# Kernel tuning notes

Hardware: AMD Instinct MI355X
Metric: run time of the kernel (lower is better)

Reference implementation:

```python
import jax, jax.numpy as jnp
import numpy as np

DIM = 128
NUM_HEADS = 4
SPLIT_SIZE = 8
HEAD_DIM = DIM // NUM_HEADS
SCALE = HEAD_DIM ** -0.5


def setup_inputs() -> dict:
    key = jax.random.key(0)
    qkv = jax.random.normal(key, (3, 8, 4096, DIM), dtype=jnp.float32)
    return {"qkv": qkv, "H": 64, "W": 64}


def _to_windows(x, H, W, H_sp, W_sp):
    # x: [B, L, C] -> [B*nW, num_heads, H_sp*W_sp, head_dim]
    B, L, C = x.shape
    x = x.reshape(B, H // H_sp, H_sp, W // W_sp, W_sp, C)
    x = x.transpose(0, 1, 3, 2, 4, 5).reshape(-1, H_sp * W_sp, NUM_HEADS, C // NUM_HEADS)
    return x.transpose(0, 2, 1, 3)


def reference(qkv, H, W):
    # idx=0 branch: vertical strips, H_sp = H (full height), W_sp = split_size
    H_sp, W_sp = H, SPLIT_SIZE
    B, L, C = qkv.shape[1], qkv.shape[2], qkv.shape[3]
    q = _to_windows(qkv[0], H, W, H_sp, W_sp) * SCALE
    k = _to_windows(qkv[1], H, W, H_sp, W_sp)
    v = _to_windows(qkv[2], H, W, H_sp, W_sp)
    # [nW, h, S, S] with S = H_sp*W_sp
    attn = jax.nn.softmax(jnp.einsum('whqd,whkd->whqk', q, k), axis=-1)
    x = jnp.einsum('whqk,whkd->whqd', attn, v)
    # merge heads: [nW, S, C]
    x = x.transpose(0, 2, 1, 3).reshape(-1, H_sp * W_sp, C)
    # windows2img: [B, H*W, C]
    x = x.reshape(B, H // H_sp, W // W_sp, H_sp, W_sp, C)
    x = x.transpose(0, 1, 3, 2, 4, 5).reshape(B, H * W, C)
    return x
```

## Files before the change

kernel.cpp:

```cpp
#include <hip/hip_runtime.h>


typedef __attribute__((ext_vector_type(8)))  short bf16x8;
typedef __attribute__((ext_vector_type(4)))  float f32x4;
typedef __attribute__((ext_vector_type(16))) float f32x16;
typedef __attribute__((ext_vector_type(4)))  int   i32x4;

#define MFMA32(a, b, c) __builtin_amdgcn_mfma_f32_32x32x16_bf16(a, b, c, 0, 0, 0)

__device__ __forceinline__ unsigned cvtpk(float lo, float hi) {
    unsigned r;
    asm("v_cvt_pk_bf16_f32 %0, %1, %2" : "=v"(r) : "v"(lo), "v"(hi));
    return r;
}
__device__ __forceinline__ void plswap(unsigned& a, unsigned& b) {
    asm("v_permlane32_swap_b32 %0, %1" : "+v"(a), "+v"(b));
}

__global__ __launch_bounds__(256, 4)
void lepe_attn_r8(const float* __restrict__ qkv, float* __restrict__ out)
{
    __shared__ __align__(16) short    Ks[256 * 32];
    __shared__ __align__(16) unsigned Vt32[32 * 132];

    const int tid  = threadIdx.x;
    const int wave = tid >> 6;
    const int lane = tid & 63;
    const int m31  = lane & 31;
    const int hi   = lane >> 5;

    const int blk  = blockIdx.x;
    const int pair = blk >> 2;
    const int qsp  = blk & 3;
    const int wi   = pair >> 2;
    const int hd   = pair & 3;
    const int b    = wi >> 3;
    const int wb   = wi & 7;
    const int chead = hd * 32;

    const size_t baseQ = (size_t)b * 524288;
    const size_t baseK = baseQ + 8u * 524288;
    const size_t baseV = baseQ + 16u * 524288;

    const int q0w = qsp * 128 + wave * 32;
    const float QS = 0.17677669529663687f * 1.4426950408889634f;
    bf16x8 qf0, qf1;
    {
        int qg = q0w + m31;
        int lq = (qg >> 3) * 64 + wb * 8 + (qg & 7);
        const float* qp = qkv + baseQ + (size_t)lq * 128 + chead + hi * 8;
        f32x4 qa = *(const f32x4*)qp;
        f32x4 qb = *(const f32x4*)(qp + 4);
        f32x4 qc = *(const f32x4*)(qp + 16);
        f32x4 qd = *(const f32x4*)(qp + 20);
        i32x4 w0, w1;
        w0[0] = cvtpk(qa[0] * QS, qa[1] * QS);
        w0[1] = cvtpk(qa[2] * QS, qa[3] * QS);
        w0[2] = cvtpk(qb[0] * QS, qb[1] * QS);
        w0[3] = cvtpk(qb[2] * QS, qb[3] * QS);
        w1[0] = cvtpk(qc[0] * QS, qc[1] * QS);
        w1[1] = cvtpk(qc[2] * QS, qc[3] * QS);
        w1[2] = cvtpk(qd[0] * QS, qd[1] * QS);
        w1[3] = cvtpk(qd[2] * QS, qd[3] * QS);
        qf0 = __builtin_bit_cast(bf16x8, w0);
        qf1 = __builtin_bit_cast(bf16x8, w1);
    }

    f32x16 o = (f32x16)0.0f;
    float lsum = 0.0f;

    const short* Vts = (const short*)Vt32;

    for (int stage = 0; stage < 2; ++stage) {
        if (stage) __syncthreads();
        const int keybase = stage * 256;

#pragma unroll
        for (int i = 0; i < 4; ++i) {
            int chunk = i * 256 + tid;
            int row   = chunk >> 2;
            int part  = chunk & 3;
            int gk    = keybase + row;
            int lk    = (gk >> 3) * 64 + wb * 8 + (gk & 7);
            const float* kp = qkv + baseK + (size_t)lk * 128 + chead + part * 8;
            f32x4 k0 = *(const f32x4*)kp;
            f32x4 k1 = *(const f32x4*)(kp + 4);
            i32x4 kd;
            kd[0] = cvtpk(k0[0], k0[1]);
            kd[1] = cvtpk(k0[2], k0[3]);
            kd[2] = cvtpk(k1[0], k1[1]);
            kd[3] = cvtpk(k1[2], k1[3]);
            *(i32x4*)&Ks[row * 32 + ((part ^ ((row >> 1) & 3)) << 3)] = kd;
        }
        {
            int p    = tid >> 1;
            int half = tid & 1;
            int k0g  = keybase + 2 * p;
            int l0   = (k0g >> 3) * 64 + wb * 8 + (k0g & 7);
            const float* va = qkv + baseV + (size_t)l0 * 128 + chead + half * 16;
            const float* vb = va + 128;
            f32x4 a[4], bb[4];
#pragma unroll
            for (int j = 0; j < 4; ++j) { a[j] = *(const f32x4*)(va + 4 * j); bb[j] = *(const f32x4*)(vb + 4 * j); }
#pragma unroll
            for (int j = 0; j < 4; ++j)
#pragma unroll
                for (int e = 0; e < 4; ++e) {
                    int dim = half * 16 + j * 4 + e;
                    Vt32[dim * 132 + p] = cvtpk(a[j][e], bb[j][e]);
                }
        }
        __syncthreads();

        for (int kb = 0; kb < 256; kb += 32) {
            int row0 = kb + m31;
            int swz  = (row0 >> 1) & 3;
            bf16x8 kfa = *(const bf16x8*)&Ks[row0 * 32 + (((0 + hi) ^ swz) << 3)];
            bf16x8 kfb = *(const bf16x8*)&Ks[row0 * 32 + (((2 + hi) ^ swz) << 3)];
            bf16x8 vf0 = *(const bf16x8*)&Vts[m31 * 264 + kb + hi * 8];
            bf16x8 vf1 = *(const bf16x8*)&Vts[m31 * 264 + kb + 16 + hi * 8];

            f32x16 s = MFMA32(kfa, qf0, (f32x16)0.0f);
            s = MFMA32(kfb, qf1, s);

            float p[16];
#pragma unroll
            for (int r = 0; r < 16; ++r) p[r] = __builtin_amdgcn_exp2f(s[r]);

            float t01 = p[0] + p[1],   t23 = p[2] + p[3];
            float t45 = p[4] + p[5],   t67 = p[6] + p[7];
            float t89 = p[8] + p[9],   tab = p[10] + p[11];
            float tcd = p[12] + p[13], tef = p[14] + p[15];
            lsum += ((t01 + t23) + (t45 + t67)) + ((t89 + tab) + (tcd + tef));

            unsigned c0 = cvtpk(p[0], p[1]);
            unsigned c1 = cvtpk(p[2], p[3]);
            unsigned c2 = cvtpk(p[4], p[5]);
            unsigned c3 = cvtpk(p[6], p[7]);
            plswap(c0, c2);
            plswap(c1, c3);
            i32x4 pw0; pw0[0] = c0; pw0[1] = c1; pw0[2] = c2; pw0[3] = c3;

            unsigned c4 = cvtpk(p[8], p[9]);
            unsigned c5 = cvtpk(p[10], p[11]);
            unsigned c6 = cvtpk(p[12], p[13]);
            unsigned c7 = cvtpk(p[14], p[15]);
            plswap(c4, c6);
            plswap(c5, c7);
            i32x4 pw1; pw1[0] = c4; pw1[1] = c5; pw1[2] = c6; pw1[3] = c7;

            o = MFMA32(__builtin_bit_cast(bf16x8, pw0), vf0, o);
            o = MFMA32(__builtin_bit_cast(bf16x8, pw1), vf1, o);
        }
    }

    float ls  = lsum + __shfl_xor(lsum, 32);
    float inv = 1.0f / ls;
    const size_t baseO = (size_t)b * 524288;
#pragma unroll
    for (int r = 0; r < 16; ++r) {
        int qw = (r & 3) + 8 * (r >> 2) + 4 * hi;
        float iv = __shfl(inv, qw);
        int q  = q0w + qw;
        int lq = (q >> 3) * 64 + wb * 8 + (q & 7);
        out[baseO + (size_t)lq * 128 + chead + m31] = o[r] * iv;
    }
}

extern "C" void kernel_launch(void* const* d_in, const int* in_sizes, int n_in,
                              void* d_out, int out_size, void* d_ws, size_t ws_size,
                              hipStream_t stream) {
    const float* qkv = (const float*)d_in[0];
    float* out = (float*)d_out;
    lepe_attn_r8<<<dim3(1024), dim3(256), 0, stream>>>(qkv, out);
}
```

Before: 104.2 us.

## Merge four query-split blocks into one 1024-thread block sharing K/V tiles

The four blocks that handled different query quarters of the same window and head become one 1024-thread block of 16 waves. K and V for that window-head are now loaded from global memory, converted to bf16 and staged in shared memory once instead of four times, with the staging loops reshaped so each thread does less copying. The cost is larger blocks: 256 blocks, about one per CU, with every wave waiting at one block-wide barrier. The launch bound of 1024 threads and 4 blocks may also force a tight register budget and cause spills.

```diff
diff --git a/kernel.cpp b/kernel.cpp
--- a/kernel.cpp
+++ b/kernel.cpp
@@ -17,8 +17,8 @@
     asm("v_permlane32_swap_b32 %0, %1" : "+v"(a), "+v"(b));
 }
 
-__global__ __launch_bounds__(256, 4)
-void lepe_attn_r8(const float* __restrict__ qkv, float* __restrict__ out)
+__global__ __launch_bounds__(1024, 4)
+void lepe_attn_r9(const float* __restrict__ qkv, float* __restrict__ out)
 {
     __shared__ __align__(16) short    Ks[256 * 32];
     __shared__ __align__(16) unsigned Vt32[32 * 132];
@@ -29,9 +29,7 @@
     const int m31  = lane & 31;
     const int hi   = lane >> 5;
 
-    const int blk  = blockIdx.x;
-    const int pair = blk >> 2;
-    const int qsp  = blk & 3;
+    const int pair = blockIdx.x;
     const int wi   = pair >> 2;
     const int hd   = pair & 3;
     const int b    = wi >> 3;
@@ -42,7 +40,9 @@
     const size_t baseK = baseQ + 8u * 524288;
     const size_t baseV = baseQ + 16u * 524288;
 
-    const int q0w = qsp * 128 + wave * 32;
+    const int qsp = wave >> 2;
+    const int wv  = wave & 3;
+    const int q0w = qsp * 128 + wv * 32;
     const float QS = 0.17677669529663687f * 1.4426950408889634f;
     bf16x8 qf0, qf1;
     {
@@ -75,13 +75,11 @@
         if (stage) __syncthreads();
         const int keybase = stage * 256;
 
-#pragma unroll
-        for (int i = 0; i < 4; ++i) {
-            int chunk = i * 256 + tid;
-            int row   = chunk >> 2;
-            int part  = chunk & 3;
-            int gk    = keybase + row;
-            int lk    = (gk >> 3) * 64 + wb * 8 + (gk & 7);
+        {
+            int row  = tid >> 2;
+            int part = tid & 3;
+            int gk   = keybase + row;
+            int lk   = (gk >> 3) * 64 + wb * 8 + (gk & 7);
             const float* kp = qkv + baseK + (size_t)lk * 128 + chead + part * 8;
             f32x4 k0 = *(const f32x4*)kp;
             f32x4 k1 = *(const f32x4*)(kp + 4);
@@ -93,22 +91,16 @@
             *(i32x4*)&Ks[row * 32 + ((part ^ ((row >> 1) & 3)) << 3)] = kd;
         }
         {
-            int p    = tid >> 1;
-            int half = tid & 1;
-            int k0g  = keybase + 2 * p;
-            int l0   = (k0g >> 3) * 64 + wb * 8 + (k0g & 7);
-            const float* va = qkv + baseV + (size_t)l0 * 128 + chead + half * 16;
-            const float* vb = va + 128;
-            f32x4 a[4], bb[4];
+            int p  = tid & 127;
+            int qd = tid >> 7;
+            int k0g = keybase + 2 * p;
+            int l0  = (k0g >> 3) * 64 + wb * 8 + (k0g & 7);
+            const float* va = qkv + baseV + (size_t)l0 * 128 + chead + qd * 4;
+            f32x4 a  = *(const f32x4*)va;
+            f32x4 bbv = *(const f32x4*)(va + 128);
 #pragma unroll
-            for (int j = 0; j < 4; ++j) { a[j] = *(const f32x4*)(va + 4 * j); bb[j] = *(const f32x4*)(vb + 4 * j); }
-#pragma unroll
-            for (int j = 0; j < 4; ++j)
-#pragma unroll
-                for (int e = 0; e < 4; ++e) {
-                    int dim = half * 16 + j * 4 + e;
-                    Vt32[dim * 132 + p] = cvtpk(a[j][e], bb[j][e]);
-                }
+            for (int e = 0; e < 4; ++e)
+                Vt32[(qd * 4 + e) * 132 + p] = cvtpk(a[e], bbv[e]);
         }
         __syncthreads();
 
@@ -172,5 +164,5 @@
                               hipStream_t stream) {
     const float* qkv = (const float*)d_in[0];
     float* out = (float*)d_out;
-    lepe_attn_r8<<<dim3(1024), dim3(256), 0, stream>>>(qkv, out);
+    lepe_attn_r9<<<dim3(256), dim3(1024), 0, stream>>>(qkv, out);
 }
```

Result: slower. 110.4 us (+6.0%).
